# Kernel optimization log

Hardware: AMD Instinct MI355X
Metric: run time of the kernel (lower is better)

## Reference

```python
import jax, jax.numpy as jnp
import numpy as np

EPS = 1e-6

def elu_plus_one(x):
    # F.elu(x) + 1 == exp(x) for x<=0, x+1 for x>0
    return jnp.where(x > 0, x + 1.0, jnp.exp(jnp.minimum(x, 0.0)))

def setup_inputs() -> dict:
    key = jax.random.key(0)
    k1, k2, k3, k4, k5 = jax.random.split(key, 5)
    B, S, D, M = 2, 4096, 1024, 4
    queries = jax.random.normal(k1, (B, S, D), dtype=jnp.float32)
    keys = jax.random.normal(k2, (B, S, D), dtype=jnp.float32)
    values = jax.random.normal(k3, (B, S, D), dtype=jnp.float32)
    # small-scale warm memory state; norms positive (accumulated sigma(k) sums)
    memories = jax.random.normal(k4, (M, D, D), dtype=jnp.float32) * 0.02
    memory_norms = jax.random.uniform(k5, (M, D), dtype=jnp.float32)
    return {"queries": queries, "keys": keys, "values": values,
            "memories": memories, "memory_norms": memory_norms}

def reference(queries, keys, values, memories, memory_norms):
    B, S, D = queries.shape
    M = memories.shape[0]

    # ---------------- retrieve ----------------
    sigma_q = elu_plus_one(queries)                                   # (B,S,D)
    a_mem = jnp.einsum('bsd,mde->mbse', sigma_q, memories)            # (M,B,S,D)
    qnorm = jnp.einsum('bsd,md->mbs', sigma_q, memory_norms)          # (M,B,S)
    outputs = a_mem / jnp.clip(qnorm, EPS, None)[..., None]           # (M,B,S,D)
    # relevance: sigma(Q) @ landmark, mean over seq -> (M,B)
    rel = qnorm.mean(axis=-1)
    empty = jnp.sum(jnp.abs(memory_norms), axis=1) < EPS              # (M,)
    NEG = jnp.float32(-1e30)
    rel = jnp.where(empty[:, None], NEG, rel)
    weights = jax.nn.softmax(rel, axis=0)                             # (M,B)
    outputs = jnp.where(empty[:, None, None, None], 0.0, outputs)
    out = jnp.einsum('mbsd,mb->bsd', outputs, weights)
    # if every slot empty, torch returns zeros
    out = jnp.where(jnp.all(empty), jnp.zeros_like(out), out)

    # ---------------- update (delta rule, current_idx = 0) ----------------
    sigma_k = elu_plus_one(keys)                                      # (B,S,D)
    mem0, norm0 = memories[0], memory_norms[0]
    retrieved_unnorm = jnp.matmul(sigma_k, mem0)                      # (B,S,D)
    knorm = jnp.clip(jnp.matmul(sigma_k, norm0), EPS, None)[..., None]
    delta_v = values - retrieved_unnorm / knorm
    mem_update = jnp.einsum('bsd,bse->de', sigma_k, delta_v) / (B * S)
    new_memory = jax.lax.stop_gradient(mem0 + mem_update)             # .detach()
    new_memory_norm = jax.lax.stop_gradient(norm0 + sigma_k.sum(axis=(0, 1)) / B)
    return out, new_memory, new_memory_norm
```

## Files before the change

kernel.cpp:

```cpp
#include <hip/hip_runtime.h>
#include <math.h>

#define B_ 2
#define S_ 4096
#define D_ 1024
#define M_ 4
#define N_ (B_*S_)
#define EPS 1e-6f

typedef unsigned short u16;
typedef __bf16 bf16x8 __attribute__((ext_vector_type(8)));
typedef float  f32x4  __attribute__((ext_vector_type(4)));

__device__ __forceinline__ float elu1(float x) {
    return x > 0.0f ? x + 1.0f : __expf(x);
}

__device__ __forceinline__ u16 f2b(float f) {
    unsigned int u = __float_as_uint(f);
    return (u16)((u + 0x7FFFu + ((u >> 16) & 1u)) >> 16);
}

#define GLDS16(gp, lp) __builtin_amdgcn_global_load_lds( \
    (const __attribute__((address_space(1))) void*)(gp), \
    (__attribute__((address_space(3))) void*)(lp), 16, 0, 0)

__global__ __launch_bounds__(256) void k1_stats(
    const float* __restrict__ Q, const float* __restrict__ mnorm,
    float* __restrict__ qnorm,
    u16* __restrict__ sQ,
    float* __restrict__ knorm, float* __restrict__ colsum)
{
    int r = blockIdx.x;
    int t = threadIdx.x;
    if (r < 32) {
        knorm[r * 256 + t] = 0.0f;
        if (r < 4) colsum[r * 256 + t] = 0.0f;
    }
    float4 q4 = *(const float4*)(Q + (size_t)r * D_ + t * 4);
    float sq0 = elu1(q4.x), sq1 = elu1(q4.y), sq2 = elu1(q4.z), sq3 = elu1(q4.w);

    uint2 sv;
    sv.x = (unsigned)f2b(sq0) | ((unsigned)f2b(sq1) << 16);
    sv.y = (unsigned)f2b(sq2) | ((unsigned)f2b(sq3) << 16);
    *(uint2*)(sQ + (size_t)r * D_ + t * 4) = sv;

    float vals[M_];
    #pragma unroll
    for (int m = 0; m < M_; ++m) {
        float4 w4 = *(const float4*)(mnorm + m * D_ + t * 4);
        vals[m] = sq0 * w4.x + sq1 * w4.y + sq2 * w4.z + sq3 * w4.w;
    }

    __shared__ float sbuf[M_][4];
    int wave = t >> 6, lane = t & 63;
    #pragma unroll
    for (int i = 0; i < M_; ++i) {
        float v = vals[i];
        #pragma unroll
        for (int off = 32; off > 0; off >>= 1) v += __shfl_down(v, off, 64);
        if (lane == 0) sbuf[i][wave] = v;
    }
    __syncthreads();
    if (t == 0) {
        #pragma unroll
        for (int m = 0; m < M_; ++m)
            qnorm[(size_t)m * N_ + r] = sbuf[m][0] + sbuf[m][1] + sbuf[m][2] + sbuf[m][3];
    }
}

__global__ __launch_bounds__(256) void prep_k(
    const float* __restrict__ K, const float* __restrict__ mnorm,
    u16* __restrict__ sk, u16* __restrict__ skT,
    float* __restrict__ colsum, float* __restrict__ knorm)
{
    __shared__ float tile[64][65];
    __shared__ float mn0[64];
    int r0 = blockIdx.x * 64;
    int d0 = blockIdx.y * 64;
    int t = threadIdx.x;
    int rr = t >> 4, c4 = (t & 15) * 4;
    if (t >= 128 && t < 192) mn0[t - 128] = mnorm[d0 + (t - 128)];
    #pragma unroll
    for (int i = 0; i < 4; ++i) {
        int rri = rr + i * 16;
        float4 k4 = *(const float4*)(K + (size_t)(r0 + rri) * D_ + d0 + c4);
        float e0 = elu1(k4.x), e1 = elu1(k4.y), e2 = elu1(k4.z), e3 = elu1(k4.w);
        uint2 v; v.x = (unsigned)f2b(e0) | ((unsigned)f2b(e1) << 16);
        v.y = (unsigned)f2b(e2) | ((unsigned)f2b(e3) << 16);
        *(uint2*)(sk + (size_t)(r0 + rri) * D_ + d0 + c4) = v;
        tile[rri][c4 + 0] = e0; tile[rri][c4 + 1] = e1;
        tile[rri][c4 + 2] = e2; tile[rri][c4 + 3] = e3;
    }
    __syncthreads();
    #pragma unroll
    for (int i = 0; i < 4; ++i) {
        int dd = rr + i * 16;
        float v0 = tile[c4 + 0][dd], v1 = tile[c4 + 1][dd];
        float v2 = tile[c4 + 2][dd], v3 = tile[c4 + 3][dd];
        uint2 v; v.x = (unsigned)f2b(v0) | ((unsigned)f2b(v1) << 16);
        v.y = (unsigned)f2b(v2) | ((unsigned)f2b(v3) << 16);
        *(uint2*)(skT + (size_t)(d0 + dd) * N_ + r0 + c4) = v;
    }
    if (t < 64) {
        float s = 0.0f;
        #pragma unroll
        for (int j = 0; j < 64; ++j) s += tile[t][j] * mn0[j];
        atomicAdd(&knorm[r0 + t], s);
    } else if (t < 128) {
        int c = t - 64;
        float s = 0.0f;
        #pragma unroll
        for (int j = 0; j < 64; ++j) s += tile[j][c];
        atomicAdd(&colsum[d0 + c], s);
    }
}

__global__ __launch_bounds__(256) void prep_memT(
    const float* __restrict__ Mem, u16* __restrict__ MemT,
    float* __restrict__ out_mem)
{
    __shared__ float tile[64][65];
    int m = blockIdx.z;
    int e0 = blockIdx.x * 64, d0 = blockIdx.y * 64;
    int t = threadIdx.x, rr = t >> 4, c4 = (t & 15) * 4;
    #pragma unroll
    for (int i = 0; i < 4; ++i) {
        int dd = rr + i * 16;
        float4 v4 = *(const float4*)(Mem + ((size_t)m * D_ + d0 + dd) * D_ + e0 + c4);
        tile[dd][c4 + 0] = v4.x; tile[dd][c4 + 1] = v4.y;
        tile[dd][c4 + 2] = v4.z; tile[dd][c4 + 3] = v4.w;
        if (m == 0)
            *(float4*)(out_mem + (size_t)(d0 + dd) * D_ + e0 + c4) = v4;
    }
    __syncthreads();
    #pragma unroll
    for (int i = 0; i < 4; ++i) {
        int ee = rr + i * 16;
        float v0 = tile[c4 + 0][ee], v1 = tile[c4 + 1][ee];
        float v2 = tile[c4 + 2][ee], v3 = tile[c4 + 3][ee];
        uint2 v; v.x = (unsigned)f2b(v0) | ((unsigned)f2b(v1) << 16);
        v.y = (unsigned)f2b(v2) | ((unsigned)f2b(v3) << 16);
        *(uint2*)(MemT + (size_t)(e0 + ee) * (M_ * D_) + m * D_ + d0 + c4) = v;
    }
}

__global__ __launch_bounds__(512) void k2_weights(
    const float* __restrict__ mnorm, const float* __restrict__ qnorm,
    float* __restrict__ weights)
{
    __shared__ float sbuf[12][8];
    int t = threadIdx.x, wave = t >> 6, lane = t & 63;
    float vals[12];
    #pragma unroll
    for (int m = 0; m < M_; ++m) {
        float v = 0.0f;
        for (int d = t; d < D_; d += 512) v += fabsf(mnorm[m * D_ + d]);
        vals[m] = v;
    }
    #pragma unroll
    for (int mb = 0; mb < M_ * B_; ++mb) {
        int m = mb >> 1, b = mb & 1;
        const float4* p = (const float4*)(qnorm + (size_t)m * N_ + (size_t)b * S_);
        float v = 0.0f;
        for (int i = t; i < S_ / 4; i += 512) {
            float4 x = p[i];
            v += x.x + x.y + x.z + x.w;
        }
        vals[4 + mb] = v;
    }
    #pragma unroll
    for (int i = 0; i < 12; ++i) {
        float v = vals[i];
        #pragma unroll
        for (int off = 32; off > 0; off >>= 1) v += __shfl_down(v, off, 64);
        if (lane == 0) sbuf[i][wave] = v;
    }
    __syncthreads();
    if (t == 0) {
        bool empty[M_]; bool all_empty = true;
        float relsum[M_ * B_];
        #pragma unroll
        for (int m = 0; m < M_; ++m) {
            float sa = 0.0f;
            #pragma unroll
            for (int w = 0; w < 8; ++w) sa += sbuf[m][w];
            empty[m] = (sa < EPS);
            all_empty = all_empty && empty[m];
        }
        #pragma unroll
        for (int mb = 0; mb < M_ * B_; ++mb) {
            float sv = 0.0f;
            #pragma unroll
            for (int w = 0; w < 8; ++w) sv += sbuf[4 + mb][w];
            relsum[mb] = sv;
        }
        for (int b = 0; b < B_; ++b) {
            float rel[M_]; float mx = -3.0e38f;
            #pragma unroll
            for (int m = 0; m < M_; ++m) {
                rel[m] = empty[m] ? -1.0e30f : relsum[m * B_ + b] * (1.0f / (float)S_);
                mx = fmaxf(mx, rel[m]);
            }
            float se = 0.0f;
            #pragma unroll
            for (int m = 0; m < M_; ++m) { rel[m] = __expf(rel[m] - mx); se += rel[m]; }
            #pragma unroll
            for (int m = 0; m < M_; ++m) {
                float wv = rel[m] / se;
                if (empty[m] || all_empty) wv = 0.0f;
                weights[m * B_ + b] = wv;
            }
        }
    }
}

__global__ __launch_bounds__(256) void k2_cvec(
    const float* __restrict__ qnorm, const float* __restrict__ weights,
    const float* __restrict__ mnorm, const float* __restrict__ colsum,
    float* __restrict__ ratT, float* __restrict__ norm_out)
{
    int g = blockIdx.x * 256 + threadIdx.x;
    if (g < N_) {
        int b = g / S_;
        float cs[M_];
        #pragma unroll
        for (int m = 0; m < M_; ++m)
            cs[m] = fmaxf(weights[m * B_ + b] / fmaxf(qnorm[(size_t)m * N_ + g], EPS), 1e-20f);
        ratT[0 * (size_t)N_ + g] = cs[0] / cs[1];
        ratT[1 * (size_t)N_ + g] = cs[1] / cs[2];
        ratT[2 * (size_t)N_ + g] = cs[2] / cs[3];
        ratT[3 * (size_t)N_ + g] = cs[3];
    }
    if (g < D_) norm_out[g] = mnorm[g] + colsum[g] * (1.0f / (float)B_);
}

__device__ __forceinline__ void tile_mma(
    const u16* Asb, const u16* Bsb, int aoff, int boff, f32x4 (&acc)[4][4])
{
    bf16x8 af[4], bf[4];
    #pragma unroll
    for (int i = 0; i < 4; ++i) {
        af[i] = *(const bf16x8*)((const char*)Asb + aoff + i * 1024);
        bf[i] = *(const bf16x8*)((const char*)Bsb + boff + i * 1024);
    }
    #pragma unroll
    for (int mi = 0; mi < 4; ++mi)
        #pragma unroll
        for (int ni = 0; ni < 4; ++ni)
            acc[mi][ni] = __builtin_amdgcn_mfma_f32_16x16x32_bf16(
                af[mi], bf[ni], acc[mi][ni], 0, 0, 0);
}

__device__ __forceinline__ void gemm_seg(
    u16* As, u16* Bs,
    const u16* __restrict__ A, int lda, int ak0,
    const u16* __restrict__ B, int ldb, int bk0,
    int rb, int cb, int klen,
    f32x4 (&acc)[4][4])
{
    const int tid  = threadIdx.x;
    const int lane = tid & 63;
    const int wid  = tid >> 6;
    const int wr   = wid >> 1, wc = wid & 1;
    const int r15  = lane & 15;

    const int srow0 = (wid * 2 + 0) * 16 + (lane >> 2);
    const int srow1 = (wid * 2 + 1) * 16 + (lane >> 2);
    const int sg    = ((lane & 3) ^ ((lane >> 3) & 3)) * 8;
    const u16* Ag0 = A + (size_t)(rb + srow0) * lda + ak0 + sg;
    const u16* Ag1 = A + (size_t)(rb + srow1) * lda + ak0 + sg;
    const u16* Bg0 = B + (size_t)(cb + srow0) * ldb + bk0 + sg;
    const u16* Bg1 = B + (size_t)(cb + srow1) * ldb + bk0 + sg;
    const int lo0 = (wid * 2 + 0) * 512;
    const int lo1 = (wid * 2 + 1) * 512;

    const int xo   = (((lane >> 4) ^ ((r15 >> 1) & 3)) * 16);
    const int aoff = (wr * 64 + r15) * 64 + xo;
    const int boff = (wc * 64 + r15) * 64 + xo;

    GLDS16(Ag0, As + lo0);
    GLDS16(Ag1, As + lo1);
    GLDS16(Bg0, Bs + lo0);
    GLDS16(Bg1, Bs + lo1);
    asm volatile("s_waitcnt vmcnt(0)" ::: "memory");
    __builtin_amdgcn_s_barrier();

    int cur = 0;
    for (int kt = 32; kt < klen; kt += 32) {
        int nxt = cur ^ 1;
        GLDS16(Ag0 + kt, As + nxt * 4096 + lo0);
        GLDS16(Ag1 + kt, As + nxt * 4096 + lo1);
        GLDS16(Bg0 + kt, Bs + nxt * 4096 + lo0);
        GLDS16(Bg1 + kt, Bs + nxt * 4096 + lo1);
        tile_mma(As + cur * 4096, Bs + cur * 4096, aoff, boff, acc);
        asm volatile("s_waitcnt vmcnt(0) lgkmcnt(0)" ::: "memory");
        __builtin_amdgcn_s_barrier();
        cur = nxt;
    }
    tile_mma(As + cur * 4096, Bs + cur * 4096, aoff, boff, acc);
    asm volatile("s_waitcnt lgkmcnt(0)" ::: "memory");
    __builtin_amdgcn_s_barrier();
}

__device__ __forceinline__ void epi_out(
    f32x4 (&acc)[4][4], float* __restrict__ out, int rb, int cb)
{
    int lane = threadIdx.x & 63, wid = threadIdx.x >> 6;
    int wr = wid >> 1, wc = wid & 1, r15 = lane & 15;
    #pragma unroll
    for (int mi = 0; mi < 4; ++mi) {
        int row0 = rb + wr * 64 + mi * 16 + (lane >> 4) * 4;
        #pragma unroll
        for (int ni = 0; ni < 4; ++ni) {
            int col = cb + wc * 64 + ni * 16 + r15;
            #pragma unroll
            for (int r = 0; r < 4; ++r)
                out[(size_t)(row0 + r) * D_ + col] = acc[mi][ni][r];
        }
    }
}

__device__ __forceinline__ void epi_delta(
    f32x4 (&acc)[4][4], const float* __restrict__ V,
    const float* __restrict__ knorm, u16* __restrict__ deltaT,
    int rb, int cb)
{
    int lane = threadIdx.x & 63, wid = threadIdx.x >> 6;
    int wr = wid >> 1, wc = wid & 1, r15 = lane & 15;
    #pragma unroll
    for (int mi = 0; mi < 4; ++mi) {
        int row0 = rb + wr * 64 + mi * 16 + (lane >> 4) * 4;
        float inv[4];
        #pragma unroll
        for (int r = 0; r < 4; ++r) inv[r] = 1.0f / fmaxf(knorm[row0 + r], EPS);
        #pragma unroll
        for (int ni = 0; ni < 4; ++ni) {
            int col = cb + wc * 64 + ni * 16 + r15;
            float dv[4];
            #pragma unroll
            for (int r = 0; r < 4; ++r)
                dv[r] = V[(size_t)(row0 + r) * D_ + col] - acc[mi][ni][r] * inv[r];
            uint2 pv;
            pv.x = (unsigned)f2b(dv[0]) | ((unsigned)f2b(dv[1]) << 16);
            pv.y = (unsigned)f2b(dv[2]) | ((unsigned)f2b(dv[3]) << 16);
            *(uint2*)(deltaT + (size_t)col * N_ + row0) = pv;
        }
    }
}

__global__ __launch_bounds__(256, 4) void g34_fused(
    const u16* __restrict__ sQ, const u16* __restrict__ MemT,
    const u16* __restrict__ sk, const float* __restrict__ V,
    const float* __restrict__ knorm, const float* __restrict__ ratT,
    float* __restrict__ out, u16* __restrict__ deltaT)
{
    __shared__ u16 As[2 * 4096];
    __shared__ u16 Bs[2 * 4096];
    int hw = blockIdx.x;
    int x  = hw & 7;
    int l  = hw >> 3;
    int z  = l >> 6;
    int by = l & 63, bx = x;
    int rb = by * 128, cb = bx * 128;
    int lane = threadIdx.x & 63, wid = threadIdx.x >> 6;
    int wr = wid >> 1;
    f32x4 acc[4][4];
    #pragma unroll
    for (int i = 0; i < 4; ++i)
        #pragma unroll
        for (int j = 0; j < 4; ++j) {
            f32x4 zz = {0.0f, 0.0f, 0.0f, 0.0f};
            acc[i][j] = zz;
        }
    if (z == 0) {
        #pragma unroll 1
        for (int m = 0; m < M_; ++m) {
            gemm_seg(As, Bs, sQ, D_, 0, MemT, M_ * D_, m * D_, rb, cb, D_, acc);
            const float* rp = ratT + (size_t)m * N_;
            #pragma unroll
            for (int mi = 0; mi < 4; ++mi) {
                int row0 = rb + wr * 64 + mi * 16 + (lane >> 4) * 4;
                float4 rt = *(const float4*)(rp + row0);
                #pragma unroll
                for (int ni = 0; ni < 4; ++ni) {
                    acc[mi][ni][0] *= rt.x; acc[mi][ni][1] *= rt.y;
                    acc[mi][ni][2] *= rt.z; acc[mi][ni][3] *= rt.w;
                }
            }
        }
        epi_out(acc, out, rb, cb);
    } else {
        gemm_seg(As, Bs, sk, D_, 0, MemT, M_ * D_, 0, rb, cb, D_, acc);
        epi_delta(acc, V, knorm, deltaT, rb, cb);
    }
}

#define KSPLIT 8
__global__ __launch_bounds__(256, 4) void g5_update(
    const u16* __restrict__ skT, const u16* __restrict__ deltaT,
    float* __restrict__ memout)
{
    __shared__ u16 As[2 * 4096];
    __shared__ u16 Bs[2 * 4096];
    f32x4 acc[4][4];
    #pragma unroll
    for (int i = 0; i < 4; ++i)
        #pragma unroll
        for (int j = 0; j < 4; ++j) {
            f32x4 zz = {0.0f, 0.0f, 0.0f, 0.0f};
            acc[i][j] = zz;
        }
    int rb = blockIdx.y * 128, cb = blockIdx.x * 128;
    int k0 = blockIdx.z * (N_ / KSPLIT);
    gemm_seg(As, Bs, skT, N_, k0, deltaT, N_, k0, rb, cb, N_ / KSPLIT, acc);
    int lane = threadIdx.x & 63, wid = threadIdx.x >> 6;
    int wr = wid >> 1, wc = wid & 1, r15 = lane & 15;
    const float sc = 1.0f / (float)N_;
    #pragma unroll
    for (int mi = 0; mi < 4; ++mi) {
        int row0 = rb + wr * 64 + mi * 16 + (lane >> 4) * 4;
        #pragma unroll
        for (int ni = 0; ni < 4; ++ni) {
            int col = cb + wc * 64 + ni * 16 + r15;
            #pragma unroll
            for (int r = 0; r < 4; ++r)
                atomicAdd(memout + (size_t)(row0 + r) * D_ + col, acc[mi][ni][r] * sc);
        }
    }
}

extern "C" void kernel_launch(void* const* d_in, const int* in_sizes, int n_in,
                              void* d_out, int out_size, void* d_ws, size_t ws_size,
                              hipStream_t stream) {
    const float* Q     = (const float*)d_in[0];
    const float* K     = (const float*)d_in[1];
    const float* V     = (const float*)d_in[2];
    const float* Mem   = (const float*)d_in[3];
    const float* Mnorm = (const float*)d_in[4];

    float* out      = (float*)d_out;
    float* out_mem  = out + (size_t)N_ * D_;
    float* out_norm = out_mem + (size_t)D_ * D_;

    char* wsb = (char*)d_ws;
    float* qnorm   = (float*)wsb;
    float* knorm   = qnorm + (size_t)M_ * N_;
    float* colsum  = knorm + N_;
    float* weights = colsum + D_;
    float* ratT    = weights + M_ * B_;
    u16* MemT   = (u16*)(wsb + (size_t)1  * (1 << 20));
    u16* sk     = (u16*)(wsb + (size_t)9  * (1 << 20));
    u16* skT    = (u16*)(wsb + (size_t)25 * (1 << 20));
    u16* sQ     = (u16*)(wsb + (size_t)41 * (1 << 20));
    u16* deltaT = (u16*)(wsb + (size_t)57 * (1 << 20));

    hipLaunchKernelGGL(k1_stats, dim3(N_), dim3(256), 0, stream, Q, Mnorm, qnorm, sQ, knorm, colsum);
    hipLaunchKernelGGL(prep_k, dim3(128, 16), dim3(256), 0, stream, K, Mnorm, sk, skT, colsum, knorm);
    hipLaunchKernelGGL(prep_memT, dim3(16, 16, 4), dim3(256), 0, stream, Mem, MemT, out_mem);
    hipLaunchKernelGGL(k2_weights, dim3(1), dim3(512), 0, stream, Mnorm, qnorm, weights);
    hipLaunchKernelGGL(k2_cvec, dim3(32), dim3(256), 0, stream, qnorm, weights, Mnorm, colsum, ratT, out_norm);
    hipLaunchKernelGGL(g34_fused, dim3(1024), dim3(256), 0, stream,
                       sQ, MemT, sk, V, knorm, ratT, out, deltaT);
    hipLaunchKernelGGL(g5_update, dim3(8, 8, KSPLIT), dim3(256), 0, stream, skT, deltaT, out_mem);
}
```

Before: 221.8 us.

## Enlarge g34 tiles to 256x128 with K=64 steps and 512-thread blocks

Replaces the 128x128, K=32 GEMM tiling in the fused retrieve/delta kernel with 256x128 tiles handled by 8 waves (512 threads), loading 64-wide K slices per stage through swizzled LDS. The larger tile and deeper K step are meant to reuse each B tile across more rows and halve the number of barrier/sync iterations, cutting global traffic and loop overhead. In exchange it uses more LDS per block (96 KB), halves the grid to 512 blocks, and lowers the occupancy target in launch bounds, which may reduce latency hiding or leave the tail of the grid unbalanced.

```diff
diff --git a/kernel.cpp b/kernel.cpp
--- a/kernel.cpp
+++ b/kernel.cpp
@@ -303,6 +303,94 @@
     __builtin_amdgcn_s_barrier();
 }
 
+__device__ __forceinline__ void mma_tile8(
+    const u16* Asb, const u16* Bsb, int arow, int brow,
+    int s0, int s1, f32x4 (&acc)[4][4])
+{
+    bf16x8 af[4], bf[4];
+    #pragma unroll
+    for (int mi = 0; mi < 4; ++mi)
+        af[mi] = *(const bf16x8*)((const char*)Asb + arow + mi * 2048 + s0);
+    #pragma unroll
+    for (int ni = 0; ni < 4; ++ni)
+        bf[ni] = *(const bf16x8*)((const char*)Bsb + brow + ni * 2048 + s0);
+    #pragma unroll
+    for (int mi = 0; mi < 4; ++mi)
+        #pragma unroll
+        for (int ni = 0; ni < 4; ++ni)
+            acc[mi][ni] = __builtin_amdgcn_mfma_f32_16x16x32_bf16(
+                af[mi], bf[ni], acc[mi][ni], 0, 0, 0);
+    #pragma unroll
+    for (int mi = 0; mi < 4; ++mi)
+        af[mi] = *(const bf16x8*)((const char*)Asb + arow + mi * 2048 + s1);
+    #pragma unroll
+    for (int ni = 0; ni < 4; ++ni)
+        bf[ni] = *(const bf16x8*)((const char*)Bsb + brow + ni * 2048 + s1);
+    #pragma unroll
+    for (int mi = 0; mi < 4; ++mi)
+        #pragma unroll
+        for (int ni = 0; ni < 4; ++ni)
+            acc[mi][ni] = __builtin_amdgcn_mfma_f32_16x16x32_bf16(
+                af[mi], bf[ni], acc[mi][ni], 0, 0, 0);
+}
+
+__device__ __forceinline__ void gemm_seg8(
+    u16* As, u16* Bs,
+    const u16* __restrict__ A, int lda, int ak0,
+    const u16* __restrict__ B, int ldb, int bk0,
+    int rb, int cb, int klen,
+    f32x4 (&acc)[4][4])
+{
+    const int tid  = threadIdx.x;
+    const int lane = tid & 63;
+    const int wid  = tid >> 6;
+    const int wr   = wid >> 1, wc = wid & 1;
+    const int r15  = lane & 15;
+
+    const int sg = (((lane & 7) ^ (lane >> 3)) * 8);
+    const int rA = tid >> 3;
+    const u16* Ag0 = A + (size_t)(rb +   0 + rA) * lda + ak0 + sg;
+    const u16* Ag1 = A + (size_t)(rb +  64 + rA) * lda + ak0 + sg;
+    const u16* Ag2 = A + (size_t)(rb + 128 + rA) * lda + ak0 + sg;
+    const u16* Ag3 = A + (size_t)(rb + 192 + rA) * lda + ak0 + sg;
+    const u16* Bg0 = B + (size_t)(cb +   0 + rA) * ldb + bk0 + sg;
+    const u16* Bg1 = B + (size_t)(cb +  64 + rA) * ldb + bk0 + sg;
+    const int lw = wid * 512;
+
+    const int arow = (wr * 64 + r15) * 128;
+    const int brow = (wc * 64 + r15) * 128;
+    const int g4 = lane >> 4, l7 = lane & 7;
+    const int s0 = ((g4) ^ l7) * 16;
+    const int s1 = ((4 + g4) ^ l7) * 16;
+
+    GLDS16(Ag0, As + 0 * 4096 + lw);
+    GLDS16(Ag1, As + 1 * 4096 + lw);
+    GLDS16(Ag2, As + 2 * 4096 + lw);
+    GLDS16(Ag3, As + 3 * 4096 + lw);
+    GLDS16(Bg0, Bs + 0 * 4096 + lw);
+    GLDS16(Bg1, Bs + 1 * 4096 + lw);
+    asm volatile("s_waitcnt vmcnt(0)" ::: "memory");
+    __builtin_amdgcn_s_barrier();
+
+    int cur = 0;
+    for (int kt = 64; kt < klen; kt += 64) {
+        int nb = cur ^ 1;
+        GLDS16(Ag0 + kt, As + nb * 16384 + 0 * 4096 + lw);
+        GLDS16(Ag1 + kt, As + nb * 16384 + 1 * 4096 + lw);
+        GLDS16(Ag2 + kt, As + nb * 16384 + 2 * 4096 + lw);
+        GLDS16(Ag3 + kt, As + nb * 16384 + 3 * 4096 + lw);
+        GLDS16(Bg0 + kt, Bs + nb * 8192 + 0 * 4096 + lw);
+        GLDS16(Bg1 + kt, Bs + nb * 8192 + 1 * 4096 + lw);
+        mma_tile8(As + cur * 16384, Bs + cur * 8192, arow, brow, s0, s1, acc);
+        asm volatile("s_waitcnt vmcnt(0) lgkmcnt(0)" ::: "memory");
+        __builtin_amdgcn_s_barrier();
+        cur = nb;
+    }
+    mma_tile8(As + cur * 16384, Bs + cur * 8192, arow, brow, s0, s1, acc);
+    asm volatile("s_waitcnt lgkmcnt(0)" ::: "memory");
+    __builtin_amdgcn_s_barrier();
+}
+
 __device__ __forceinline__ void epi_out(
     f32x4 (&acc)[4][4], float* __restrict__ out, int rb, int cb)
 {
@@ -349,20 +437,15 @@
     }
 }
 
-__global__ __launch_bounds__(256, 4) void g34_fused(
+__global__ __launch_bounds__(512, 2) void g34_fused(
     const u16* __restrict__ sQ, const u16* __restrict__ MemT,
     const u16* __restrict__ sk, const float* __restrict__ V,
     const float* __restrict__ knorm, const float* __restrict__ ratT,
     float* __restrict__ out, u16* __restrict__ deltaT)
 {
-    __shared__ u16 As[2 * 4096];
-    __shared__ u16 Bs[2 * 4096];
+    __shared__ u16 As[2 * 16384];
+    __shared__ u16 Bs[2 * 8192];
     int hw = blockIdx.x;
-    int x  = hw & 7;
-    int l  = hw >> 3;
-    int z  = l >> 6;
-    int by = l & 63, bx = x;
-    int rb = by * 128, cb = bx * 128;
     int lane = threadIdx.x & 63, wid = threadIdx.x >> 6;
     int wr = wid >> 1;
     f32x4 acc[4][4];
@@ -373,10 +456,12 @@
             f32x4 zz = {0.0f, 0.0f, 0.0f, 0.0f};
             acc[i][j] = zz;
         }
-    if (z == 0) {
+    if (hw < 256) {
+        int bx = hw & 7, by = hw >> 3;
+        int rb = by * 256, cb = bx * 128;
         #pragma unroll 1
         for (int m = 0; m < M_; ++m) {
-            gemm_seg(As, Bs, sQ, D_, 0, MemT, M_ * D_, m * D_, rb, cb, D_, acc);
+            gemm_seg8(As, Bs, sQ, D_, 0, MemT, M_ * D_, m * D_, rb, cb, D_, acc);
             const float* rp = ratT + (size_t)m * N_;
             #pragma unroll
             for (int mi = 0; mi < 4; ++mi) {
@@ -391,7 +476,10 @@
         }
         epi_out(acc, out, rb, cb);
     } else {
-        gemm_seg(As, Bs, sk, D_, 0, MemT, M_ * D_, 0, rb, cb, D_, acc);
+        int d = hw - 256;
+        int bx = d & 7, by = d >> 3;
+        int rb = by * 256, cb = bx * 128;
+        gemm_seg8(As, Bs, sk, D_, 0, MemT, M_ * D_, 0, rb, cb, D_, acc);
         epi_delta(acc, V, knorm, deltaT, rb, cb);
     }
 }
@@ -460,7 +548,7 @@
     hipLaunchKernelGGL(prep_memT, dim3(16, 16, 4), dim3(256), 0, stream, Mem, MemT, out_mem);
     hipLaunchKernelGGL(k2_weights, dim3(1), dim3(512), 0, stream, Mnorm, qnorm, weights);
     hipLaunchKernelGGL(k2_cvec, dim3(32), dim3(256), 0, stream, qnorm, weights, Mnorm, colsum, ratT, out_norm);
-    hipLaunchKernelGGL(g34_fused, dim3(1024), dim3(256), 0, stream,
+    hipLaunchKernelGGL(g34_fused, dim3(512), dim3(512), 0, stream,
                        sQ, MemT, sk, V, knorm, ratT, out, deltaT);
     hipLaunchKernelGGL(g5_update, dim3(8, 8, KSPLIT), dim3(256), 0, stream, skT, deltaT, out_mem);
 }
```

Result: slower. 262.4 us (+18.3%).
